# Kernel optimization log

Measured on AMD Instinct MI355X. Metric: run time of the kernel, lower is better.

Reference implementation:

```python
import jax, jax.numpy as jnp
import numpy as np

N, D_IN, D_OUT, E = 4096, 4096, 4096, 8

def setup_inputs() -> dict:
    key = jax.random.key(0)
    k1, k2, k3 = jax.random.split(key, 3)
    scale_in = 1.0 / np.sqrt(D_IN)
    x = jax.random.normal(k1, (N, D_IN), dtype=jnp.float32)
    gate_w = jax.random.normal(k2, (D_IN, E), dtype=jnp.float32) * scale_in
    gate_b = jnp.zeros((E,), dtype=jnp.float32)
    expert_w = jax.random.normal(k3, (E, D_IN, D_OUT), dtype=jnp.float32) * scale_in
    expert_b = jnp.zeros((E, D_OUT), dtype=jnp.float32)
    return {"x": x, "gate_w": gate_w, "gate_b": gate_b,
            "expert_w": expert_w, "expert_b": expert_b}

def reference(x, gate_w, gate_b, expert_w, expert_b):
    # gate scores: [N, E]
    gate = jax.nn.softmax(x @ gate_w + gate_b, axis=-1)
    # all experts run on every token: [E, N, D_OUT]
    expert_out = jnp.einsum('nd,edr->enr', x, expert_w) + expert_b[:, None, :]
    # gate-weighted combine: [N, D_OUT]
    out = jnp.einsum('ne,enr->nr', gate, expert_out)
    return out
```

## Files before the change

### kernel.cpp

```cpp
#include <hip/hip_runtime.h>
#include <hip/hip_bf16.h>


typedef __attribute__((ext_vector_type(8))) short short8;
typedef __attribute__((ext_vector_type(4))) float f32x4;

#define NROWS 4096
#define DIN   4096
#define DOUT  4096
#define NEXP  8
#define KTOT  (NEXP * DIN)

__device__ __forceinline__ unsigned short f2b(float f) {
  unsigned int u = __float_as_uint(f);
  u += 0x7FFFu + ((u >> 16) & 1u);
  return (unsigned short)(u >> 16);
}

__device__ __forceinline__ void gload_lds16(const unsigned short* g, unsigned short* l) {
  __builtin_amdgcn_global_load_lds(
      (const __attribute__((address_space(1))) unsigned int*)(unsigned long long)g,
      (__attribute__((address_space(3))) unsigned int*)(unsigned int)(unsigned long long)l,
      16, 0, 0);
}

__global__ __launch_bounds__(256) void gate_kernel(const float* __restrict__ x,
                                                   const float* __restrict__ gw,
                                                   const float* __restrict__ gb,
                                                   float* __restrict__ g,
                                                   unsigned short* __restrict__ xb) {
  __shared__ float red[256][8];
  const int n = blockIdx.x, t = threadIdx.x;
  float a[8] = {0, 0, 0, 0, 0, 0, 0, 0};
  for (int d = t; d < DIN; d += 256) {
    float xv = x[(size_t)n * DIN + d];
    xb[(size_t)n * DIN + d] = f2b(xv);
    const float4* gwp = (const float4*)(gw + (size_t)d * 8);
    float4 w0 = gwp[0], w1 = gwp[1];
    a[0] += xv * w0.x; a[1] += xv * w0.y; a[2] += xv * w0.z; a[3] += xv * w0.w;
    a[4] += xv * w1.x; a[5] += xv * w1.y; a[6] += xv * w1.z; a[7] += xv * w1.w;
  }
  for (int e = 0; e < 8; ++e) red[t][e] = a[e];
  __syncthreads();
  for (int s = 128; s > 0; s >>= 1) {
    if (t < s)
      for (int e = 0; e < 8; ++e) red[t][e] += red[t + s][e];
    __syncthreads();
  }
  if (t == 0) {
    float l[8], m = -1e30f, ssum = 0.f;
    for (int e = 0; e < 8; ++e) { l[e] = red[0][e] + gb[e]; m = fmaxf(m, l[e]); }
    for (int e = 0; e < 8; ++e) { l[e] = expf(l[e] - m); ssum += l[e]; }
    for (int e = 0; e < 8; ++e) g[(size_t)n * 8 + e] = l[e] / ssum;
  }
}

__global__ __launch_bounds__(256) void transpose_w(const float* __restrict__ W,
                                                   unsigned short* __restrict__ bt) {
  __shared__ unsigned short tile[64][72];
  const int t = threadIdx.x;
  const int k0 = blockIdx.x * 64, r0 = blockIdx.y * 64;
  #pragma unroll
  for (int i = 0; i < 4; ++i) {
    int lin = i * 256 + t;
    int kr = lin >> 4, rq = (lin & 15) * 4;
    float4 v = *(const float4*)(W + (size_t)(k0 + kr) * 4096 + r0 + rq);
    tile[rq + 0][kr] = f2b(v.x);
    tile[rq + 1][kr] = f2b(v.y);
    tile[rq + 2][kr] = f2b(v.z);
    tile[rq + 3][kr] = f2b(v.w);
  }
  __syncthreads();
  #pragma unroll
  for (int i = 0; i < 2; ++i) {
    int lin = i * 256 + t;
    int rr = lin >> 3, kc = (lin & 7) * 8;
    uint4 v = *(const uint4*)&tile[rr][kc];
    *(uint4*)(bt + (size_t)(r0 + rr) * KTOT + k0 + kc) = v;
  }
}

#define BM 256
#define BN 256
#define BKK 32
#define NTILES (KTOT / BKK)
#define SLOT_SH 8192

__global__ __launch_bounds__(512, 2) void gemm_moe(const unsigned short* __restrict__ xb,
                                                   const unsigned short* __restrict__ bt,
                                                   const float* __restrict__ gate,
                                                   const float* __restrict__ eb,
                                                   float* __restrict__ out) {
  __shared__ alignas(16) unsigned short sA[4 * SLOT_SH];
  __shared__ alignas(16) unsigned short sB[4 * SLOT_SH];
  __shared__ float sG[256 * 8];
  __shared__ float sBias[8 * 256];

  const int t = threadIdx.x;
  const int lane = t & 63;
  const int w = t >> 6;
  const int wm = w >> 2;
  const int wn = w & 3;

  const int bid = blockIdx.x;
  const int wg = (bid & 7) * 32 + (bid >> 3);
  const int tn = wg >> 4;
  const int tm = wg & 15;
  const int row0 = tm * BM;
  const int col0 = tn * BN;

  #pragma unroll
  for (int i = 0; i < 4; ++i) {
    int lin = i * 512 + t;
    sG[lin] = gate[(size_t)row0 * 8 + lin];
    sBias[lin] = eb[(size_t)(lin >> 8) * DOUT + col0 + (lin & 255)];
  }

  const int mrow = lane & 15;
  const int quad = lane >> 4;
  const int rs = (quad ^ ((mrow >> 1) & 3)) * 8;

  f32x4 acc[8][4];
  #pragma unroll
  for (int i = 0; i < 8; ++i)
    #pragma unroll
    for (int j = 0; j < 4; ++j) acc[i][j] = (f32x4){0.f, 0.f, 0.f, 0.f};

  auto stage = [&](int T, int s) {
    const int kA = (T * BKK) & (DIN - 1);
    const int kB = T * BKK;
    #pragma unroll
    for (int r = 0; r < 2; ++r) {
      const int row = r * 128 + w * 16 + (lane >> 2);
      const int srcg = (lane & 3) ^ ((row >> 1) & 3);
      gload_lds16(xb + (size_t)(row0 + row) * DIN + kA + srcg * 8,
                  &sA[s * SLOT_SH + (r * 512 + w * 64) * 8]);
      gload_lds16(bt + (size_t)(col0 + row) * KTOT + kB + srcg * 8,
                  &sB[s * SLOT_SH + (r * 512 + w * 64) * 8]);
    }
  };

  stage(0, 0);
  stage(1, 1);
  asm volatile("s_waitcnt vmcnt(4)" ::: "memory");
  __builtin_amdgcn_s_barrier();

  for (int T = 0; T < NTILES; ++T) {
    const int s = T & 3;

    if (T < NTILES - 2) stage(T + 2, (T + 2) & 3);

    short8 af[8], bf[4];
    #pragma unroll
    for (int i = 0; i < 8; ++i) {
      const int row = wm * 128 + i * 16 + mrow;
      af[i] = *(const short8*)&sA[s * SLOT_SH + row * 32 + rs];
    }
    #pragma unroll
    for (int j = 0; j < 4; ++j) {
      const int row = wn * 64 + j * 16 + mrow;
      bf[j] = *(const short8*)&sB[s * SLOT_SH + row * 32 + rs];
    }

    __builtin_amdgcn_s_setprio(1);
    #pragma unroll
    for (int i = 0; i < 8; ++i)
      #pragma unroll
      for (int j = 0; j < 4; ++j)
        acc[i][j] = __builtin_amdgcn_mfma_f32_16x16x32_bf16(af[i], bf[j], acc[i][j], 0, 0, 0);
    __builtin_amdgcn_s_setprio(0);

    if (T < NTILES - 1) {
      if (T < NTILES - 2) asm volatile("s_waitcnt vmcnt(4)" ::: "memory");
      else                asm volatile("s_waitcnt vmcnt(0)" ::: "memory");
      __builtin_amdgcn_s_barrier();

      if ((T & 127) == 127) {
        const int e = T >> 7;
        #pragma unroll
        for (int i = 0; i < 8; ++i) {
          #pragma unroll
          for (int r = 0; r < 4; ++r) {
            const int row_l = wm * 128 + i * 16 + quad * 4 + r;
            const float sc = sG[row_l * 8 + e] / sG[row_l * 8 + e + 1];
            #pragma unroll
            for (int j = 0; j < 4; ++j) acc[i][j][r] *= sc;
          }
        }
      }
    }
  }

  #pragma unroll
  for (int i = 0; i < 8; ++i) {
    #pragma unroll
    for (int r = 0; r < 4; ++r) {
      const int row_l = wm * 128 + i * 16 + quad * 4 + r;
      float gv[8];
      #pragma unroll
      for (int e = 0; e < 8; ++e) gv[e] = sG[row_l * 8 + e];
      #pragma unroll
      for (int j = 0; j < 4; ++j) {
        const int col_l = wn * 64 + j * 16 + mrow;
        float bias = 0.f;
        #pragma unroll
        for (int e = 0; e < 8; ++e) bias += gv[e] * sBias[e * 256 + col_l];
        out[(size_t)(row0 + row_l) * DOUT + col0 + col_l] = acc[i][j][r] * gv[7] + bias;
      }
    }
  }
}

__global__ __launch_bounds__(256) void moe_fallback(const float* __restrict__ x,
                                                    const float* __restrict__ gw,
                                                    const float* __restrict__ gb,
                                                    const float* __restrict__ W,
                                                    const float* __restrict__ eb,
                                                    float* __restrict__ out) {
  __shared__ float sX[64][33];
  __shared__ float sW[32][65];
  __shared__ float sLog[64][8];
  __shared__ float sGate[64][8];
  const int t = threadIdx.x;
  const int r0 = blockIdx.y * 64, c0 = blockIdx.x * 64;

  const int grow = t & 63, epair = t >> 6;
  float lg0 = gb[2 * epair], lg1 = gb[2 * epair + 1];
  for (int d0 = 0; d0 < DIN; d0 += 32) {
    for (int i = 0; i < 8; ++i) {
      int lin = i * 256 + t, rr = lin >> 5, cc = lin & 31;
      sX[rr][cc] = x[(size_t)(r0 + rr) * DIN + d0 + cc];
    }
    __syncthreads();
    for (int dd = 0; dd < 32; ++dd) {
      float xv = sX[grow][dd];
      lg0 += xv * gw[(size_t)(d0 + dd) * 8 + 2 * epair];
      lg1 += xv * gw[(size_t)(d0 + dd) * 8 + 2 * epair + 1];
    }
    __syncthreads();
  }
  sLog[grow][2 * epair] = lg0;
  sLog[grow][2 * epair + 1] = lg1;
  __syncthreads();
  if (t < 64) {
    float m = -1e30f, s = 0.f, ex[8];
    for (int e = 0; e < 8; ++e) m = fmaxf(m, sLog[t][e]);
    for (int e = 0; e < 8; ++e) { ex[e] = expf(sLog[t][e] - m); s += ex[e]; }
    for (int e = 0; e < 8; ++e) sGate[t][e] = ex[e] / s;
  }
  __syncthreads();

  const int tr = t >> 4, tc = t & 15;
  float acc[4][4] = {};
  for (int e = 0; e < NEXP; ++e) {
    float part[4][4] = {};
    for (int d0 = 0; d0 < DIN; d0 += 32) {
      for (int i = 0; i < 8; ++i) {
        int lin = i * 256 + t, rr = lin >> 5, cc = lin & 31;
        sX[rr][cc] = x[(size_t)(r0 + rr) * DIN + d0 + cc];
      }
      for (int i = 0; i < 8; ++i) {
        int lin = i * 256 + t, dd = lin >> 6, cc = lin & 63;
        sW[dd][cc] = W[(size_t)e * DIN * DOUT + (size_t)(d0 + dd) * DOUT + c0 + cc];
      }
      __syncthreads();
      for (int dd = 0; dd < 32; ++dd) {
        float xa[4], wb[4];
        for (int i = 0; i < 4; ++i) xa[i] = sX[tr + 16 * i][dd];
        for (int j = 0; j < 4; ++j) wb[j] = sW[dd][tc + 16 * j];
        for (int i = 0; i < 4; ++i)
          for (int j = 0; j < 4; ++j) part[i][j] += xa[i] * wb[j];
      }
      __syncthreads();
    }
    for (int i = 0; i < 4; ++i) {
      float g = sGate[tr + 16 * i][e];
      for (int j = 0; j < 4; ++j)
        acc[i][j] += g * (part[i][j] + eb[(size_t)e * DOUT + c0 + tc + 16 * j]);
    }
  }
  for (int i = 0; i < 4; ++i)
    for (int j = 0; j < 4; ++j)
      out[(size_t)(r0 + tr + 16 * i) * DOUT + c0 + tc + 16 * j] = acc[i][j];
}

extern "C" void kernel_launch(void* const* d_in, const int* in_sizes, int n_in,
                              void* d_out, int out_size, void* d_ws, size_t ws_size,
                              hipStream_t stream) {
  const float* x  = (const float*)d_in[0];
  const float* gw = (const float*)d_in[1];
  const float* gb = (const float*)d_in[2];
  const float* W  = (const float*)d_in[3];
  const float* eb = (const float*)d_in[4];
  float* out = (float*)d_out;

  const size_t sz_xb = (size_t)NROWS * DIN * 2;
  const size_t sz_bt = (size_t)DOUT * KTOT * 2;
  const size_t sz_g  = (size_t)NROWS * 8 * 4;
  const size_t need = sz_xb + sz_bt + sz_g;

  if (ws_size >= need) {
    unsigned short* xb = (unsigned short*)d_ws;
    unsigned short* bt = (unsigned short*)((char*)d_ws + sz_xb);
    float* gate = (float*)((char*)d_ws + sz_xb + sz_bt);
    gate_kernel<<<NROWS, 256, 0, stream>>>(x, gw, gb, gate, xb);
    transpose_w<<<dim3(KTOT / 64, DOUT / 64), 256, 0, stream>>>(W, bt);
    gemm_moe<<<(NROWS / BM) * (DOUT / BN), 512, 0, stream>>>(xb, bt, gate, eb, out);
  } else {
    moe_fallback<<<dim3(DOUT / 64, NROWS / 64), 256, 0, stream>>>(x, gw, gb, W, eb, out);
  }
}
```

Baseline: 1.748 ms.

## Split GEMM main loop into two phases interleaving loads with MFMA

The GEMM inner loop is split into two halves. A-tile prefetch is issued during the first MFMA batch and B-tile prefetch during the second, with extra barriers so waves stay in lockstep, in a ping-pong style schedule. Separately, the gate kernel is vectorized with float4 loads and uses wave shuffles instead of an LDS tree reduction, and the weight transpose uses an XOR-swizzled LDS tile instead of padding. The extra barriers per iteration could add sync overhead, while the gate and transpose changes target the smaller prep kernels.

```diff
diff --git a/kernel.cpp b/kernel.cpp
--- a/kernel.cpp
+++ b/kernel.cpp
@@ -29,27 +29,40 @@
                                                    const float* __restrict__ gb,
                                                    float* __restrict__ g,
                                                    unsigned short* __restrict__ xb) {
-  __shared__ float red[256][8];
+  __shared__ float red[4][8];
   const int n = blockIdx.x, t = threadIdx.x;
+  const int lane = t & 63, w = t >> 6;
   float a[8] = {0, 0, 0, 0, 0, 0, 0, 0};
-  for (int d = t; d < DIN; d += 256) {
-    float xv = x[(size_t)n * DIN + d];
-    xb[(size_t)n * DIN + d] = f2b(xv);
-    const float4* gwp = (const float4*)(gw + (size_t)d * 8);
-    float4 w0 = gwp[0], w1 = gwp[1];
-    a[0] += xv * w0.x; a[1] += xv * w0.y; a[2] += xv * w0.z; a[3] += xv * w0.w;
-    a[4] += xv * w1.x; a[5] += xv * w1.y; a[6] += xv * w1.z; a[7] += xv * w1.w;
-  }
-  for (int e = 0; e < 8; ++e) red[t][e] = a[e];
+  #pragma unroll
+  for (int it = 0; it < DIN / 1024; ++it) {
+    const int d = (it * 256 + t) * 4;
+    float4 xv = *(const float4*)(x + (size_t)n * DIN + d);
+    ushort4 p;
+    p.x = f2b(xv.x); p.y = f2b(xv.y); p.z = f2b(xv.z); p.w = f2b(xv.w);
+    *(ushort4*)(xb + (size_t)n * DIN + d) = p;
+    const float xs[4] = {xv.x, xv.y, xv.z, xv.w};
+    #pragma unroll
+    for (int q = 0; q < 4; ++q) {
+      const float4* gwp = (const float4*)(gw + (size_t)(d + q) * 8);
+      float4 w0 = gwp[0], w1 = gwp[1];
+      a[0] += xs[q] * w0.x; a[1] += xs[q] * w0.y; a[2] += xs[q] * w0.z; a[3] += xs[q] * w0.w;
+      a[4] += xs[q] * w1.x; a[5] += xs[q] * w1.y; a[6] += xs[q] * w1.z; a[7] += xs[q] * w1.w;
+    }
+  }
+  #pragma unroll
+  for (int off = 32; off; off >>= 1)
+    #pragma unroll
+    for (int e = 0; e < 8; ++e) a[e] += __shfl_xor(a[e], off);
+  if (lane == 0)
+    #pragma unroll
+    for (int e = 0; e < 8; ++e) red[w][e] = a[e];
   __syncthreads();
-  for (int s = 128; s > 0; s >>= 1) {
-    if (t < s)
-      for (int e = 0; e < 8; ++e) red[t][e] += red[t + s][e];
-    __syncthreads();
-  }
   if (t == 0) {
     float l[8], m = -1e30f, ssum = 0.f;
-    for (int e = 0; e < 8; ++e) { l[e] = red[0][e] + gb[e]; m = fmaxf(m, l[e]); }
+    for (int e = 0; e < 8; ++e) {
+      l[e] = red[0][e] + red[1][e] + red[2][e] + red[3][e] + gb[e];
+      m = fmaxf(m, l[e]);
+    }
     for (int e = 0; e < 8; ++e) { l[e] = expf(l[e] - m); ssum += l[e]; }
     for (int e = 0; e < 8; ++e) g[(size_t)n * 8 + e] = l[e] / ssum;
   }
@@ -57,26 +70,34 @@
 
 __global__ __launch_bounds__(256) void transpose_w(const float* __restrict__ W,
                                                    unsigned short* __restrict__ bt) {
-  __shared__ unsigned short tile[64][72];
+  __shared__ unsigned short tile[64 * 64];
   const int t = threadIdx.x;
   const int k0 = blockIdx.x * 64, r0 = blockIdx.y * 64;
   #pragma unroll
   for (int i = 0; i < 4; ++i) {
     int lin = i * 256 + t;
-    int kr = lin >> 4, rq = (lin & 15) * 4;
-    float4 v = *(const float4*)(W + (size_t)(k0 + kr) * 4096 + r0 + rq);
-    tile[rq + 0][kr] = f2b(v.x);
-    tile[rq + 1][kr] = f2b(v.y);
-    tile[rq + 2][kr] = f2b(v.z);
-    tile[rq + 3][kr] = f2b(v.w);
+    int kr = lin >> 4;
+    int G = lin & 15;
+    float4 v = *(const float4*)(W + (size_t)(k0 + kr) * 4096 + r0 + G * 4);
+    int slot = G ^ (kr & 15) ^ ((kr >> 4) & 3);
+    ushort4 p;
+    p.x = f2b(v.x); p.y = f2b(v.y); p.z = f2b(v.z); p.w = f2b(v.w);
+    *(ushort4*)&tile[kr * 64 + slot * 4] = p;
   }
   __syncthreads();
   #pragma unroll
   for (int i = 0; i < 2; ++i) {
     int lin = i * 256 + t;
-    int rr = lin >> 3, kc = (lin & 7) * 8;
-    uint4 v = *(const uint4*)&tile[rr][kc];
-    *(uint4*)(bt + (size_t)(r0 + rr) * KTOT + k0 + kc) = v;
+    int rr = lin >> 3;
+    int kc = (lin & 7) * 8;
+    unsigned short buf[8];
+    #pragma unroll
+    for (int j = 0; j < 8; ++j) {
+      int k = kc + j;
+      int slot = (rr >> 2) ^ (k & 15) ^ ((k >> 4) & 3);
+      buf[j] = tile[k * 64 + slot * 4 + (rr & 3)];
+    }
+    *(uint4*)(bt + (size_t)(r0 + rr) * KTOT + k0 + kc) = *(uint4*)buf;
   }
 }
 
@@ -120,54 +141,75 @@
   const int quad = lane >> 4;
   const int rs = (quad ^ ((mrow >> 1) & 3)) * 8;
 
+  const int srow = w * 16 + (lane >> 2);
+  const int sg0 = (lane & 3) ^ ((srow >> 1) & 3);
+  const int sg1 = (lane & 3) ^ (((srow + 128) >> 1) & 3);
+
   f32x4 acc[8][4];
   #pragma unroll
   for (int i = 0; i < 8; ++i)
     #pragma unroll
     for (int j = 0; j < 4; ++j) acc[i][j] = (f32x4){0.f, 0.f, 0.f, 0.f};
 
-  auto stage = [&](int T, int s) {
+  auto stageA = [&](int T) {
+    const int s = T & 3;
     const int kA = (T * BKK) & (DIN - 1);
+    gload_lds16(xb + (size_t)(row0 + srow) * DIN + kA + sg0 * 8,
+                &sA[s * SLOT_SH + (w * 64) * 8]);
+    gload_lds16(xb + (size_t)(row0 + 128 + srow) * DIN + kA + sg1 * 8,
+                &sA[s * SLOT_SH + (512 + w * 64) * 8]);
+  };
+  auto stageB = [&](int T) {
+    const int s = T & 3;
     const int kB = T * BKK;
-    #pragma unroll
-    for (int r = 0; r < 2; ++r) {
-      const int row = r * 128 + w * 16 + (lane >> 2);
-      const int srcg = (lane & 3) ^ ((row >> 1) & 3);
-      gload_lds16(xb + (size_t)(row0 + row) * DIN + kA + srcg * 8,
-                  &sA[s * SLOT_SH + (r * 512 + w * 64) * 8]);
-      gload_lds16(bt + (size_t)(col0 + row) * KTOT + kB + srcg * 8,
-                  &sB[s * SLOT_SH + (r * 512 + w * 64) * 8]);
-    }
+    gload_lds16(bt + (size_t)(col0 + srow) * KTOT + kB + sg0 * 8,
+                &sB[s * SLOT_SH + (w * 64) * 8]);
+    gload_lds16(bt + (size_t)(col0 + 128 + srow) * KTOT + kB + sg1 * 8,
+                &sB[s * SLOT_SH + (512 + w * 64) * 8]);
   };
 
-  stage(0, 0);
-  stage(1, 1);
+  stageA(0); stageB(0);
+  stageA(1); stageB(1);
   asm volatile("s_waitcnt vmcnt(4)" ::: "memory");
   __builtin_amdgcn_s_barrier();
 
   for (int T = 0; T < NTILES; ++T) {
     const int s = T & 3;
-
-    if (T < NTILES - 2) stage(T + 2, (T + 2) & 3);
-
-    short8 af[8], bf[4];
-    #pragma unroll
-    for (int i = 0; i < 8; ++i) {
-      const int row = wm * 128 + i * 16 + mrow;
-      af[i] = *(const short8*)&sA[s * SLOT_SH + row * 32 + rs];
-    }
-    #pragma unroll
-    for (int j = 0; j < 4; ++j) {
-      const int row = wn * 64 + j * 16 + mrow;
-      bf[j] = *(const short8*)&sB[s * SLOT_SH + row * 32 + rs];
-    }
-
+    const unsigned short* sAs = &sA[s * SLOT_SH];
+    const unsigned short* sBs = &sB[s * SLOT_SH];
+
+    short8 af0[4], bf[4];
+    #pragma unroll
+    for (int i = 0; i < 4; ++i)
+      af0[i] = *(const short8*)&sAs[(wm * 128 + i * 16 + mrow) * 32 + rs];
+    #pragma unroll
+    for (int j = 0; j < 4; ++j)
+      bf[j] = *(const short8*)&sBs[(wn * 64 + j * 16 + mrow) * 32 + rs];
+    if (T < NTILES - 2) stageA(T + 2);
+    __builtin_amdgcn_s_barrier();
+    asm volatile("s_waitcnt lgkmcnt(0)" ::: "memory");
     __builtin_amdgcn_s_setprio(1);
     #pragma unroll
-    for (int i = 0; i < 8; ++i)
+    for (int i = 0; i < 4; ++i)
       #pragma unroll
       for (int j = 0; j < 4; ++j)
-        acc[i][j] = __builtin_amdgcn_mfma_f32_16x16x32_bf16(af[i], bf[j], acc[i][j], 0, 0, 0);
+        acc[i][j] = __builtin_amdgcn_mfma_f32_16x16x32_bf16(af0[i], bf[j], acc[i][j], 0, 0, 0);
+    __builtin_amdgcn_s_setprio(0);
+    __builtin_amdgcn_s_barrier();
+
+    short8 af1[4];
+    #pragma unroll
+    for (int i = 0; i < 4; ++i)
+      af1[i] = *(const short8*)&sAs[(wm * 128 + (4 + i) * 16 + mrow) * 32 + rs];
+    if (T < NTILES - 2) stageB(T + 2);
+    __builtin_amdgcn_s_barrier();
+    asm volatile("s_waitcnt lgkmcnt(0)" ::: "memory");
+    __builtin_amdgcn_s_setprio(1);
+    #pragma unroll
+    for (int i = 0; i < 4; ++i)
+      #pragma unroll
+      for (int j = 0; j < 4; ++j)
+        acc[4 + i][j] = __builtin_amdgcn_mfma_f32_16x16x32_bf16(af1[i], bf[j], acc[4 + i][j], 0, 0, 0);
     __builtin_amdgcn_s_setprio(0);
 
     if (T < NTILES - 1) {
```

After: 1.804 ms. 3.2% more time.
